# Performance work log

Hardware: AMD Instinct MI355X
Metric: run time of the kernel (lower is better)

## Reference

```python
import jax, jax.numpy as jnp
import numpy as np

B, S, H = 4, 2048, 1024
NH = 16
HD = H // NH  # 64
EPS = 1e-12


def setup_inputs() -> dict:
    key = jax.random.key(0)
    ks = jax.random.split(key, 10)
    sc = 1.0 / np.sqrt(H)
    return {
        "hidden_states": jax.random.normal(ks[0], (B, S, H), jnp.float32),
        "attention_mask": jnp.ones((B, S), jnp.float32),
        "Wq": jax.random.normal(ks[1], (H, H), jnp.float32) * sc,
        "bq": jnp.zeros((H,), jnp.float32),
        "Wk": jax.random.normal(ks[2], (H, H), jnp.float32) * sc,
        "bk": jnp.zeros((H,), jnp.float32),
        "Wv": jax.random.normal(ks[3], (H, H), jnp.float32) * sc,
        "bv": jnp.zeros((H,), jnp.float32),
        "Wd": jax.random.normal(ks[4], (H, H), jnp.float32) * sc,
        "bd": jnp.zeros((H,), jnp.float32),
        "ln_g": jnp.ones((H,), jnp.float32),
        "ln_b": jnp.zeros((H,), jnp.float32),
    }


def reference(hidden_states, attention_mask, Wq, bq, Wk, bk, Wv, bv, Wd, bd, ln_g, ln_b):
    def heads(x):  # [B,S,H] -> [B,NH,S,HD]
        return x.reshape(B, S, NH, HD).transpose(0, 2, 1, 3)

    q = heads(hidden_states @ Wq.T + bq)
    k = heads(hidden_states @ Wk.T + bk)
    v = heads(hidden_states @ Wv.T + bv)

    scores = jnp.einsum('bhqd,bhkd->bhqk', q, k) / np.sqrt(HD).astype(np.float32)
    # 2D mask -> [B,1,1,S]; (1-m)*-10000 additive bias
    bias = (1.0 - attention_mask)[:, None, None, :] * -10000.0
    probs = jax.nn.softmax(scores + bias, axis=-1)  # dropout p=0 -> identity

    ctx = jnp.einsum('bhqk,bhkd->bhqd', probs, v)
    ctx = ctx.transpose(0, 2, 1, 3).reshape(B, S, H)

    out = ctx @ Wd.T + bd
    x = out + hidden_states
    mu = jnp.mean(x, axis=-1, keepdims=True)
    var = jnp.mean(jnp.square(x - mu), axis=-1, keepdims=True)
    return (x - mu) * jax.lax.rsqrt(var + EPS) * ln_g + ln_b
```

## Files before the change

kernel.cpp:

```cpp
#include <hip/hip_runtime.h>
#include <stdint.h>

#define B_ 4
#define S_ 2048
#define H_ 1024
#define NH_ 16
#define HD_ 64

typedef __bf16 bf16x8 __attribute__((ext_vector_type(8)));
typedef unsigned short u16x8 __attribute__((ext_vector_type(8)));
typedef float f32x4 __attribute__((ext_vector_type(4)));
typedef float f32x16 __attribute__((ext_vector_type(16)));

__device__ __forceinline__ unsigned short f2bf(float x) {
  union { float f; unsigned u; } c; c.f = x;
  unsigned r = (c.u + 0x7FFFu + ((c.u >> 16) & 1u)) >> 16;
  return (unsigned short)r;
}

__device__ __forceinline__ unsigned cvtpk(float lo, float hi) {
  unsigned r;
  asm("v_cvt_pk_bf16_f32 %0, %1, %2" : "=v"(r) : "v"(lo), "v"(hi));
  return r;
}

__device__ __forceinline__ void gload16(const unsigned short* g, unsigned short* lds) {
  __builtin_amdgcn_global_load_lds((const __attribute__((address_space(1))) void*)g,
                                   (__attribute__((address_space(3))) void*)lds, 16, 0, 0);
}

__global__ __launch_bounds__(256) void cvt_kernel(const float* __restrict__ src,
                                                  unsigned short* __restrict__ dst, int n) {
  int i = (blockIdx.x * blockDim.x + threadIdx.x) * 4;
  if (i < n) {
    float4 v = *reinterpret_cast<const float4*>(src + i);
    ushort4 o;
    o.x = f2bf(v.x); o.y = f2bf(v.y); o.z = f2bf(v.z); o.w = f2bf(v.w);
    *reinterpret_cast<ushort4*>(dst + i) = o;
  }
}

__global__ __launch_bounds__(256) void cvtw_kernel(const float* __restrict__ w0,
                                                   const float* __restrict__ w1,
                                                   const float* __restrict__ w2,
                                                   const float* __restrict__ w3,
                                                   unsigned short* __restrict__ o0,
                                                   unsigned short* __restrict__ o1,
                                                   unsigned short* __restrict__ o2,
                                                   unsigned short* __restrict__ o3, int n) {
  const int which = blockIdx.y;
  const float* src = (which == 0) ? w0 : (which == 1) ? w1 : (which == 2) ? w2 : w3;
  unsigned short* dst = (which == 0) ? o0 : (which == 1) ? o1 : (which == 2) ? o2 : o3;
  int i = (blockIdx.x * blockDim.x + threadIdx.x) * 4;
  if (i < n) {
    float4 v = *reinterpret_cast<const float4*>(src + i);
    ushort4 o;
    o.x = f2bf(v.x); o.y = f2bf(v.y); o.z = f2bf(v.z); o.w = f2bf(v.w);
    *reinterpret_cast<ushort4*>(dst + i) = o;
  }
}

template <bool BF16OUT>
__global__ __launch_bounds__(256) void gemm_bt(const unsigned short* __restrict__ A,
                                               const unsigned short* __restrict__ Bm,
                                               const float* __restrict__ bias,
                                               void* __restrict__ Cout,
                                               int M, int N, int K) {
  __shared__ unsigned short As[128 * 32];
  __shared__ unsigned short Bs[128 * 32];
  const int t = threadIdx.x;
  const int lane = t & 63;
  const int wv = t >> 6;
  const int wm = wv >> 1, wn = wv & 1;
  const int m0 = blockIdx.x * 128, n0 = blockIdx.y * 128;
  const int l15 = lane & 15, g8 = (lane >> 4) * 8;

  f32x4 acc[4][4];
#pragma unroll
  for (int i = 0; i < 4; ++i)
#pragma unroll
    for (int j = 0; j < 4; ++j) { f32x4 z = {0.f, 0.f, 0.f, 0.f}; acc[i][j] = z; }

  const int rowA = t >> 2;
  const int colA = (t & 3) * 8;
  const unsigned short* gA0 = A + (long)(m0 + rowA) * K + colA;
  const unsigned short* gA1 = A + (long)(m0 + 64 + rowA) * K + colA;
  const unsigned short* gB0 = Bm + (long)(n0 + rowA) * K + colA;
  const unsigned short* gB1 = Bm + (long)(n0 + 64 + rowA) * K + colA;
  unsigned short* ldsA0 = &As[wv * 512];
  unsigned short* ldsA1 = &As[2048 + wv * 512];
  unsigned short* ldsB0 = &Bs[wv * 512];
  unsigned short* ldsB1 = &Bs[2048 + wv * 512];

  for (int k0 = 0; k0 < K; k0 += 32) {
    __syncthreads();
    gload16(gA0 + k0, ldsA0);
    gload16(gA1 + k0, ldsA1);
    gload16(gB0 + k0, ldsB0);
    gload16(gB1 + k0, ldsB1);
    __syncthreads();

    bf16x8 af[4], bfr[4];
#pragma unroll
    for (int i = 0; i < 4; ++i)
      af[i] = *reinterpret_cast<const bf16x8*>(&As[(wm * 64 + i * 16 + l15) * 32 + g8]);
#pragma unroll
    for (int j = 0; j < 4; ++j)
      bfr[j] = *reinterpret_cast<const bf16x8*>(&Bs[(wn * 64 + j * 16 + l15) * 32 + g8]);
#pragma unroll
    for (int i = 0; i < 4; ++i)
#pragma unroll
      for (int j = 0; j < 4; ++j)
        acc[i][j] = __builtin_amdgcn_mfma_f32_16x16x32_bf16(af[i], bfr[j], acc[i][j], 0, 0, 0);
  }

  const int r0 = (lane >> 4) * 4;
#pragma unroll
  for (int i = 0; i < 4; ++i)
#pragma unroll
    for (int j = 0; j < 4; ++j) {
      int col = n0 + wn * 64 + j * 16 + l15;
      float bv = bias[col];
#pragma unroll
      for (int r = 0; r < 4; ++r) {
        int row = m0 + wm * 64 + i * 16 + r0 + r;
        float v = acc[i][j][r] + bv;
        if (BF16OUT)
          ((unsigned short*)Cout)[(long)row * N + col] = f2bf(v);
        else
          ((float*)Cout)[(long)row * N + col] = v;
      }
    }
}

__global__ __launch_bounds__(256, 4) void attn_kernel(const unsigned short* __restrict__ Q,
                                                      const unsigned short* __restrict__ Kg,
                                                      const unsigned short* __restrict__ Vg,
                                                      const float* __restrict__ mask,
                                                      unsigned short* __restrict__ ctx) {
  __shared__ __align__(16) unsigned short Kt[2][64 * 72];
  __shared__ __align__(16) unsigned short VtT[2][64 * 72];
  __shared__ __align__(16) float biasL[2][64];
  __shared__ __align__(16) float alBuf[4][32];
  __shared__ int mflag[2];
  __shared__ int anyMsh;

  const int t = threadIdx.x, lane = t & 63;
  const int wv = t >> 6;
  const int h = blockIdx.y, b = blockIdx.z;
  const int q0w = blockIdx.x * 128 + wv * 32;
  const int l31 = lane & 31, h2 = lane >> 5;
  const long headoff = (long)h * HD_;
  const float L2E = 1.44269504088896f;
  const float SC = 0.125f * L2E;

  if (t == 0) anyMsh = 0;
  __syncthreads();
  {
    bool nz = false;
    for (int i = t; i < S_; i += 256) nz |= (mask[(long)b * S_ + i] != 1.0f);
    if (__any(nz) && lane == 0) atomicOr(&anyMsh, 1);
  }

  bf16x8 qf[4];
  {
    const unsigned short* Qrow = Q + ((long)(b * S_ + q0w + l31)) * H_ + headoff;
#pragma unroll
    for (int c = 0; c < 4; ++c) {
      bf16x8 raw = *reinterpret_cast<const bf16x8*>(Qrow + 16 * c + 8 * h2);
#pragma unroll
      for (int j = 0; j < 8; ++j) qf[c][j] = (__bf16)((float)raw[j] * SC);
    }
  }
  __syncthreads();
  const bool anyM = (anyMsh != 0);

  f32x16 o[2];
#pragma unroll
  for (int dt = 0; dt < 2; ++dt)
#pragma unroll
    for (int r = 0; r < 16; ++r) o[dt][r] = 0.f;
  float mrow = -1.0e30f, lsum = 0.f;

  const int rowd0 = l31, rowd1 = 32 + l31;
  const int grp0 = (rowd0 >> 3) & 7, grp1 = (rowd1 >> 3) & 7;

  int voff0[4], voff1[4];
#pragma unroll
  for (int kc = 0; kc < 4; ++kc) {
    voff0[kc] = rowd0 * 72 + 8 * ((2 * kc + h2) ^ grp0);
    voff1[kc] = rowd1 * 72 + 8 * ((2 * kc + h2) ^ grp1);
  }

  const int krow = t >> 3, kcg = (t & 7) * 8;
  const int vrow = (t >> 3) * 2, dc = t & 7;
  const long gbase = (long)(b * S_) * H_ + headoff;
  u16x8 kr0, kr1, vr0, vr1;

  auto LOADT = [&](int kv0) {
    kr0 = *reinterpret_cast<const u16x8*>(Kg + gbase + (long)(kv0 + krow) * H_ + kcg);
    kr1 = *reinterpret_cast<const u16x8*>(Kg + gbase + (long)(kv0 + krow + 32) * H_ + kcg);
    vr0 = *reinterpret_cast<const u16x8*>(Vg + gbase + (long)(kv0 + vrow) * H_ + dc * 8);
    vr1 = *reinterpret_cast<const u16x8*>(Vg + gbase + (long)(kv0 + vrow + 1) * H_ + dc * 8);
  };
  auto WRITET = [&](int buf, int kv0) {
    *reinterpret_cast<u16x8*>(&Kt[buf][krow * 72 + kcg]) = kr0;
    *reinterpret_cast<u16x8*>(&Kt[buf][(krow + 32) * 72 + kcg]) = kr1;
    const int pos = (vrow & 7) | (((vrow >> 3) ^ dc) << 3);
#pragma unroll
    for (int j = 0; j < 8; ++j) {
      ushort2 pr; pr.x = vr0[j]; pr.y = vr1[j];
      *reinterpret_cast<ushort2*>(&VtT[buf][(dc * 8 + j) * 72 + pos]) = pr;
    }
    if (anyM && t < 64) {
      float mv = mask[(long)b * S_ + kv0 + t];
      biasL[buf][t] = (1.f - mv) * (-10000.f * L2E);
      unsigned long long bal = __ballot(mv != 1.0f);
      if (t == 0) mflag[buf] = (bal != 0ull);
    }
  };

  auto SMPV = [&](f32x16& sv, int kvt, int cur) {
    float m0 = fmaxf(fmaxf(sv[0], sv[1]), sv[2]);
    float m1 = fmaxf(fmaxf(sv[3], sv[4]), sv[5]);
    float m2 = fmaxf(fmaxf(sv[6], sv[7]), sv[8]);
    float m3 = fmaxf(fmaxf(sv[9], sv[10]), sv[11]);
    float m4 = fmaxf(fmaxf(sv[12], sv[13]), sv[14]);
    float t0 = fmaxf(fmaxf(m0, m1), m2);
    float t1 = fmaxf(fmaxf(m3, m4), sv[15]);
    float tm = fmaxf(t0, t1);
    tm = fmaxf(tm, __shfl_xor(tm, 32));
    if (!__all(tm <= mrow + 8.0f)) {
      float mn = fmaxf(mrow, tm);
      float al = exp2f(mrow - mn);
      mrow = mn;
      lsum *= al;
      if (lane < 32) alBuf[wv][lane] = al;
      __builtin_amdgcn_wave_barrier();
#pragma unroll
      for (int m = 0; m < 4; ++m) {
        f32x4 av = *reinterpret_cast<const f32x4*>(&alBuf[wv][8 * m + 4 * h2]);
#pragma unroll
        for (int i = 0; i < 4; ++i) {
          o[0][4 * m + i] *= av[i];
          o[1][4 * m + i] *= av[i];
        }
      }
    }
#pragma unroll
    for (int r = 0; r < 16; ++r) sv[r] = exp2f(sv[r] - mrow);
    {
      float s0 = sv[0] + sv[1], s1 = sv[2] + sv[3], s2 = sv[4] + sv[5], s3 = sv[6] + sv[7];
      float s4 = sv[8] + sv[9], s5 = sv[10] + sv[11], s6 = sv[12] + sv[13], s7 = sv[14] + sv[15];
      float u0 = s0 + s1, u1 = s2 + s3, u2 = s4 + s5, u3 = s6 + s7;
      float ts = (u0 + u1) + (u2 + u3);
      ts += __shfl_xor(ts, 32);
      lsum += ts;
    }
#pragma unroll
    for (int c2 = 0; c2 < 2; ++c2) {
      const int kc = 2 * kvt + c2;
      unsigned p0 = cvtpk(sv[8 * c2 + 0], sv[8 * c2 + 1]);
      unsigned p1 = cvtpk(sv[8 * c2 + 2], sv[8 * c2 + 3]);
      unsigned p2 = cvtpk(sv[8 * c2 + 4], sv[8 * c2 + 5]);
      unsigned p3 = cvtpk(sv[8 * c2 + 6], sv[8 * c2 + 7]);
      asm("v_permlane32_swap_b32 %0, %1" : "+v"(p0), "+v"(p2));
      asm("v_permlane32_swap_b32 %0, %1" : "+v"(p1), "+v"(p3));
      union { unsigned w[4]; bf16x8 v; } fa;
      fa.w[0] = p0; fa.w[1] = p1; fa.w[2] = p2; fa.w[3] = p3;

      bf16x8 vb0 = *reinterpret_cast<const bf16x8*>(&VtT[cur][voff0[kc]]);
      bf16x8 vb1 = *reinterpret_cast<const bf16x8*>(&VtT[cur][voff1[kc]]);
      __builtin_amdgcn_s_setprio(1);
      o[0] = __builtin_amdgcn_mfma_f32_32x32x16_bf16(fa.v, vb0, o[0], 0, 0, 0);
      o[1] = __builtin_amdgcn_mfma_f32_32x32x16_bf16(fa.v, vb1, o[1], 0, 0, 0);
      __builtin_amdgcn_s_setprio(0);
    }
  };

  const int NT = S_ / 64;
  LOADT(0);
  WRITET(0, 0);
  __syncthreads();

  for (int it = 0; it < NT; ++it) {
    const int cur = it & 1;
    const bool more = (it + 1 < NT);
    if (more) LOADT((it + 1) * 64);

    const unsigned short* KtA = &Kt[cur][l31 * 72 + 8 * h2];

    f32x16 sv0, sv1;
#pragma unroll
    for (int r = 0; r < 16; ++r) { sv0[r] = 0.f; sv1[r] = 0.f; }
    __builtin_amdgcn_s_setprio(1);
#pragma unroll
    for (int c = 0; c < 4; ++c) {
      bf16x8 af = *reinterpret_cast<const bf16x8*>(KtA + 16 * c);
      sv0 = __builtin_amdgcn_mfma_f32_32x32x16_bf16(af, qf[c], sv0, 0, 0, 0);
    }
#pragma unroll
    for (int c = 0; c < 4; ++c) {
      bf16x8 af = *reinterpret_cast<const bf16x8*>(KtA + 32 * 72 + 16 * c);
      sv1 = __builtin_amdgcn_mfma_f32_32x32x16_bf16(af, qf[c], sv1, 0, 0, 0);
    }
    __builtin_amdgcn_s_setprio(0);

    if (anyM && mflag[cur]) {
#pragma unroll
      for (int m = 0; m < 4; ++m) {
        f32x4 b0 = *reinterpret_cast<const f32x4*>(&biasL[cur][8 * m + 4 * h2]);
        f32x4 b1 = *reinterpret_cast<const f32x4*>(&biasL[cur][32 + 8 * m + 4 * h2]);
#pragma unroll
        for (int i = 0; i < 4; ++i) { sv0[4 * m + i] += b0[i]; sv1[4 * m + i] += b1[i]; }
      }
    }

    SMPV(sv0, 0, cur);
    SMPV(sv1, 1, cur);

    if (more) {
      WRITET(cur ^ 1, (it + 1) * 64);
      __syncthreads();
    }
  }

  if (lane < 32) alBuf[wv][lane] = 1.0f / lsum;
  __builtin_amdgcn_wave_barrier();
  unsigned short* ctxbase = ctx + ((long)(b * S_ + q0w + 4 * h2)) * H_ + headoff + l31;
#pragma unroll
  for (int m = 0; m < 4; ++m) {
    f32x4 iv = *reinterpret_cast<const f32x4*>(&alBuf[wv][8 * m + 4 * h2]);
#pragma unroll
    for (int i = 0; i < 4; ++i) {
#pragma unroll
      for (int dt = 0; dt < 2; ++dt)
        ctxbase[(long)(8 * m + i) * H_ + dt * 32] = f2bf(o[dt][4 * m + i] * iv[i]);
    }
  }
}

__global__ __launch_bounds__(256) void ln_kernel(const float* __restrict__ proj,
                                                 const float* __restrict__ hs,
                                                 const float* __restrict__ gam,
                                                 const float* __restrict__ bet,
                                                 float* __restrict__ out) {
  const int row = blockIdx.x;
  const int t = threadIdx.x;
  const long base = (long)row * H_ + t * 4;
  float4 a = *reinterpret_cast<const float4*>(proj + base);
  float4 hv = *reinterpret_cast<const float4*>(hs + base);
  float x0 = a.x + hv.x, x1 = a.y + hv.y, x2 = a.z + hv.z, x3 = a.w + hv.w;
  float s1 = x0 + x1 + x2 + x3;
  float s2 = x0 * x0 + x1 * x1 + x2 * x2 + x3 * x3;
#pragma unroll
  for (int off = 1; off < 64; off <<= 1) {
    s1 += __shfl_xor(s1, off);
    s2 += __shfl_xor(s2, off);
  }
  __shared__ float a1[4], a2[4];
  if ((t & 63) == 0) { a1[t >> 6] = s1; a2[t >> 6] = s2; }
  __syncthreads();
  float ts1 = a1[0] + a1[1] + a1[2] + a1[3];
  float ts2 = a2[0] + a2[1] + a2[2] + a2[3];
  float mu = ts1 * (1.0f / H_);
  float var = ts2 * (1.0f / H_) - mu * mu;
  float inv = rsqrtf(var + 1e-12f);
  float4 gv = *reinterpret_cast<const float4*>(gam + t * 4);
  float4 bb = *reinterpret_cast<const float4*>(bet + t * 4);
  float4 ov;
  ov.x = (x0 - mu) * inv * gv.x + bb.x;
  ov.y = (x1 - mu) * inv * gv.y + bb.y;
  ov.z = (x2 - mu) * inv * gv.z + bb.z;
  ov.w = (x3 - mu) * inv * gv.w + bb.w;
  *reinterpret_cast<float4*>(out + base) = ov;
}

extern "C" void kernel_launch(void* const* d_in, const int* in_sizes, int n_in,
                              void* d_out, int out_size, void* d_ws, size_t ws_size,
                              hipStream_t stream) {
  const float* hs   = (const float*)d_in[0];
  const float* mask = (const float*)d_in[1];
  const float* Wq   = (const float*)d_in[2];
  const float* bq   = (const float*)d_in[3];
  const float* Wk   = (const float*)d_in[4];
  const float* bk   = (const float*)d_in[5];
  const float* Wv   = (const float*)d_in[6];
  const float* bv   = (const float*)d_in[7];
  const float* Wd   = (const float*)d_in[8];
  const float* bd   = (const float*)d_in[9];
  const float* lng  = (const float*)d_in[10];
  const float* lnb  = (const float*)d_in[11];
  float* out = (float*)d_out;

  char* ws = (char*)d_ws;
  const size_t SZ_X = (size_t)B_ * S_ * H_ * 2;
  const size_t SZ_W = (size_t)H_ * H_ * 2;
  unsigned short* Xb  = (unsigned short*)(ws);
  unsigned short* Wqb = (unsigned short*)(ws + SZ_X);
  unsigned short* Wkb = (unsigned short*)(ws + SZ_X + SZ_W);
  unsigned short* Wvb = (unsigned short*)(ws + SZ_X + 2 * SZ_W);
  unsigned short* Wdb = (unsigned short*)(ws + SZ_X + 3 * SZ_W);
  unsigned short* Qb  = (unsigned short*)(ws + SZ_X + 4 * SZ_W);
  unsigned short* Kb  = (unsigned short*)(ws + 2 * SZ_X + 4 * SZ_W);
  unsigned short* Vb  = (unsigned short*)(ws + 3 * SZ_X + 4 * SZ_W);
  unsigned short* Cxb = (unsigned short*)(ws + 4 * SZ_X + 4 * SZ_W);
  float* Proj         = (float*)(ws + 5 * SZ_X + 4 * SZ_W);

  const int NX = B_ * S_ * H_;
  const int NW = H_ * H_;

  cvt_kernel<<<NX / 1024, 256, 0, stream>>>(hs, Xb, NX);
  dim3 gw(NW / 1024, 4);
  cvtw_kernel<<<gw, 256, 0, stream>>>(Wq, Wk, Wv, Wd, Wqb, Wkb, Wvb, Wdb, NW);

  dim3 gg(B_ * S_ / 128, H_ / 128);
  gemm_bt<true><<<gg, 256, 0, stream>>>(Xb, Wqb, bq, Qb, B_ * S_, H_, H_);
  gemm_bt<true><<<gg, 256, 0, stream>>>(Xb, Wkb, bk, Kb, B_ * S_, H_, H_);
  gemm_bt<true><<<gg, 256, 0, stream>>>(Xb, Wvb, bv, Vb, B_ * S_, H_, H_);

  dim3 ga(S_ / 128, NH_, B_);
  attn_kernel<<<ga, 256, 0, stream>>>(Qb, Kb, Vb, mask, Cxb);

  gemm_bt<false><<<gg, 256, 0, stream>>>(Cxb, Wdb, bd, Proj, B_ * S_, H_, H_);

  ln_kernel<<<B_ * S_, 256, 0, stream>>>(Proj, hs, lng, lnb, out);
}
```

Baseline: 320.1 us.

## Load K tiles directly to LDS with swizzle and remap attention grid

K tiles now go straight from global memory into LDS through a gload16 helper (likely buffer-load-to-LDS), using an XOR swizzle with no padding. This removes the register staging and the separate LDS write of K. The 3D grid becomes a 1D grid with a remap that groups 8 (batch, head) pairs per block-id chunk, meant to improve K/V L2 reuse. The launch bounds drop the occupancy hint and the two QK tiles are computed in a loop, which may change register allocation and occupancy.

```diff
diff --git a/kernel.cpp b/kernel.cpp
--- a/kernel.cpp
+++ b/kernel.cpp
@@ -133,12 +133,12 @@
     }
 }
 
-__global__ __launch_bounds__(256, 4) void attn_kernel(const unsigned short* __restrict__ Q,
-                                                      const unsigned short* __restrict__ Kg,
-                                                      const unsigned short* __restrict__ Vg,
-                                                      const float* __restrict__ mask,
-                                                      unsigned short* __restrict__ ctx) {
-  __shared__ __align__(16) unsigned short Kt[2][64 * 72];
+__global__ __launch_bounds__(256) void attn_kernel(const unsigned short* __restrict__ Q,
+                                                   const unsigned short* __restrict__ Kg,
+                                                   const unsigned short* __restrict__ Vg,
+                                                   const float* __restrict__ mask,
+                                                   unsigned short* __restrict__ ctx) {
+  __shared__ __align__(16) unsigned short Kt[2][64 * 64];
   __shared__ __align__(16) unsigned short VtT[2][64 * 72];
   __shared__ __align__(16) float biasL[2][64];
   __shared__ __align__(16) float alBuf[4][32];
@@ -147,8 +147,11 @@
 
   const int t = threadIdx.x, lane = t & 63;
   const int wv = t >> 6;
-  const int h = blockIdx.y, b = blockIdx.z;
-  const int q0w = blockIdx.x * 128 + wv * 32;
+  const int id = blockIdx.x;
+  const int bh = ((id >> 7) << 3) | (id & 7);
+  const int qb = (id >> 3) & 15;
+  const int h = bh & 15, b = bh >> 4;
+  const int q0w = qb * 128 + wv * 32;
   const int l31 = lane & 31, h2 = lane >> 5;
   const long headoff = (long)h * HD_;
   const float L2E = 1.44269504088896f;
@@ -182,9 +185,12 @@
     for (int r = 0; r < 16; ++r) o[dt][r] = 0.f;
   float mrow = -1.0e30f, lsum = 0.f;
 
+  int koff[4];
+#pragma unroll
+  for (int c = 0; c < 4; ++c) koff[c] = 8 * ((2 * c + h2) ^ (l31 & 7));
+
   const int rowd0 = l31, rowd1 = 32 + l31;
   const int grp0 = (rowd0 >> 3) & 7, grp1 = (rowd1 >> 3) & 7;
-
   int voff0[4], voff1[4];
 #pragma unroll
   for (int kc = 0; kc < 4; ++kc) {
@@ -192,20 +198,24 @@
     voff1[kc] = rowd1 * 72 + 8 * ((2 * kc + h2) ^ grp1);
   }
 
-  const int krow = t >> 3, kcg = (t & 7) * 8;
+  const long gbase = (long)(b * S_) * H_ + headoff;
+
+  const unsigned short* kg0 =
+      Kg + gbase + (long)(16 * wv + (lane >> 3)) * H_ + 8 * ((lane & 7) ^ (lane >> 3));
+  const unsigned short* kg1 = kg0 + 8 * H_;
+
   const int vrow = (t >> 3) * 2, dc = t & 7;
-  const long gbase = (long)(b * S_) * H_ + headoff;
-  u16x8 kr0, kr1, vr0, vr1;
-
-  auto LOADT = [&](int kv0) {
-    kr0 = *reinterpret_cast<const u16x8*>(Kg + gbase + (long)(kv0 + krow) * H_ + kcg);
-    kr1 = *reinterpret_cast<const u16x8*>(Kg + gbase + (long)(kv0 + krow + 32) * H_ + kcg);
+  u16x8 vr0, vr1;
+
+  auto LOADK = [&](int buf, int kv0) {
+    gload16(kg0 + (long)kv0 * H_, &Kt[buf][(16 * wv) * 64]);
+    gload16(kg1 + (long)kv0 * H_, &Kt[buf][(16 * wv + 8) * 64]);
+  };
+  auto LOADV = [&](int kv0) {
     vr0 = *reinterpret_cast<const u16x8*>(Vg + gbase + (long)(kv0 + vrow) * H_ + dc * 8);
     vr1 = *reinterpret_cast<const u16x8*>(Vg + gbase + (long)(kv0 + vrow + 1) * H_ + dc * 8);
   };
-  auto WRITET = [&](int buf, int kv0) {
-    *reinterpret_cast<u16x8*>(&Kt[buf][krow * 72 + kcg]) = kr0;
-    *reinterpret_cast<u16x8*>(&Kt[buf][(krow + 32) * 72 + kcg]) = kr1;
+  auto WRITEV = [&](int buf, int kv0) {
     const int pos = (vrow & 7) | (((vrow >> 3) ^ dc) << 3);
 #pragma unroll
     for (int j = 0; j < 8; ++j) {
@@ -279,48 +289,45 @@
   };
 
   const int NT = S_ / 64;
-  LOADT(0);
-  WRITET(0, 0);
+  LOADK(0, 0);
+  LOADV(0);
+  WRITEV(0, 0);
   __syncthreads();
 
   for (int it = 0; it < NT; ++it) {
     const int cur = it & 1;
     const bool more = (it + 1 < NT);
-    if (more) LOADT((it + 1) * 64);
-
-    const unsigned short* KtA = &Kt[cur][l31 * 72 + 8 * h2];
-
-    f32x16 sv0, sv1;
-#pragma unroll
-    for (int r = 0; r < 16; ++r) { sv0[r] = 0.f; sv1[r] = 0.f; }
-    __builtin_amdgcn_s_setprio(1);
-#pragma unroll
-    for (int c = 0; c < 4; ++c) {
-      bf16x8 af = *reinterpret_cast<const bf16x8*>(KtA + 16 * c);
-      sv0 = __builtin_amdgcn_mfma_f32_32x32x16_bf16(af, qf[c], sv0, 0, 0, 0);
-    }
-#pragma unroll
-    for (int c = 0; c < 4; ++c) {
-      bf16x8 af = *reinterpret_cast<const bf16x8*>(KtA + 32 * 72 + 16 * c);
-      sv1 = __builtin_amdgcn_mfma_f32_32x32x16_bf16(af, qf[c], sv1, 0, 0, 0);
-    }
-    __builtin_amdgcn_s_setprio(0);
-
-    if (anyM && mflag[cur]) {
-#pragma unroll
-      for (int m = 0; m < 4; ++m) {
-        f32x4 b0 = *reinterpret_cast<const f32x4*>(&biasL[cur][8 * m + 4 * h2]);
-        f32x4 b1 = *reinterpret_cast<const f32x4*>(&biasL[cur][32 + 8 * m + 4 * h2]);
-#pragma unroll
-        for (int i = 0; i < 4; ++i) { sv0[4 * m + i] += b0[i]; sv1[4 * m + i] += b1[i]; }
+    if (more) {
+      LOADK(cur ^ 1, (it + 1) * 64);
+      LOADV((it + 1) * 64);
+    }
+
+#pragma unroll
+    for (int kvt = 0; kvt < 2; ++kvt) {
+      f32x16 sv;
+#pragma unroll
+      for (int r = 0; r < 16; ++r) sv[r] = 0.f;
+      const int rb = (kvt * 32 + l31) * 64;
+      __builtin_amdgcn_s_setprio(1);
+#pragma unroll
+      for (int c = 0; c < 4; ++c) {
+        bf16x8 af = *reinterpret_cast<const bf16x8*>(&Kt[cur][rb + koff[c]]);
+        sv = __builtin_amdgcn_mfma_f32_32x32x16_bf16(af, qf[c], sv, 0, 0, 0);
       }
-    }
-
-    SMPV(sv0, 0, cur);
-    SMPV(sv1, 1, cur);
+      __builtin_amdgcn_s_setprio(0);
+      if (anyM && mflag[cur]) {
+#pragma unroll
+        for (int m = 0; m < 4; ++m) {
+          f32x4 bb = *reinterpret_cast<const f32x4*>(&biasL[cur][kvt * 32 + 8 * m + 4 * h2]);
+#pragma unroll
+          for (int i = 0; i < 4; ++i) sv[4 * m + i] += bb[i];
+        }
+      }
+      SMPV(sv, kvt, cur);
+    }
 
     if (more) {
-      WRITET(cur ^ 1, (it + 1) * 64);
+      WRITEV(cur ^ 1, (it + 1) * 64);
       __syncthreads();
     }
   }
@@ -419,8 +426,7 @@
   gemm_bt<true><<<gg, 256, 0, stream>>>(Xb, Wkb, bk, Kb, B_ * S_, H_, H_);
   gemm_bt<true><<<gg, 256, 0, stream>>>(Xb, Wvb, bv, Vb, B_ * S_, H_, H_);
 
-  dim3 ga(S_ / 128, NH_, B_);
-  attn_kernel<<<ga, 256, 0, stream>>>(Qb, Kb, Vb, mask, Cxb);
+  attn_kernel<<<dim3((S_ / 128) * NH_ * B_), 256, 0, stream>>>(Qb, Kb, Vb, mask, Cxb);
 
   gemm_bt<false><<<gg, 256, 0, stream>>>(Cxb, Wdb, bd, Proj, B_ * S_, H_, H_);
 
```

New measurement: 292.8 us. 8.5% less time.
